# Kernel optimization log

Measured on AMD Instinct MI355X. Metric: run time of the kernel, lower is better.

## Reference

```python
import jax, jax.numpy as jnp
import numpy as np
from jax import lax

# Static config (matches init_kwargs)
D_MODEL = 1024
EXPAND = 2
D_INNER = D_MODEL * EXPAND          # 2048
HEAD_DIM = 64
N_HEADS = D_INNER // HEAD_DIM       # 32
N_GROUPS = 1
D_STATE = 128
D_CONV = 4
CONV_DIM = D_INNER + 2 * N_GROUPS * D_STATE        # 2304
D_IN_PROJ = 2 * D_INNER + 2 * N_GROUPS * D_STATE + N_HEADS  # 4384
SEQLEN = 8192
LN_EPS = 1e-5


def setup_inputs() -> dict:
    key = jax.random.key(0)
    ks = jax.random.split(key, 6)
    x = jax.random.normal(ks[0], (SEQLEN, D_MODEL), jnp.float32)
    W_in = jax.random.normal(ks[1], (D_IN_PROJ, D_MODEL), jnp.float32) / np.sqrt(D_MODEL)
    W_conv = jax.random.normal(ks[2], (CONV_DIM, 1, D_CONV), jnp.float32) / np.sqrt(D_CONV)
    b_conv = jnp.zeros((CONV_DIM,), jnp.float32)
    # dt_bias init per Mamba2: dt ~ LogUniform(dt_min, dt_max), inverse-softplus
    dt = jnp.exp(jax.random.uniform(ks[3], (N_HEADS,)) * (np.log(0.1) - np.log(0.001)) + np.log(0.001))
    dt = jnp.clip(dt, 1e-4)
    dt_bias = dt + jnp.log(-jnp.expm1(-dt))
    A_log = jnp.log(jax.random.uniform(ks[4], (N_HEADS,), minval=1.0, maxval=16.0))
    D_param = jnp.ones((N_HEADS,), jnp.float32)
    ln_w = jnp.ones((D_INNER,), jnp.float32)
    ln_b = jnp.zeros((D_INNER,), jnp.float32)
    W_out = jax.random.normal(ks[5], (D_MODEL, D_INNER), jnp.float32) / np.sqrt(D_INNER)
    return dict(x=x, W_in=W_in, W_conv=W_conv, b_conv=b_conv, dt_bias=dt_bias,
                A_log=A_log, D_param=D_param, ln_w=ln_w, ln_b=ln_b, W_out=W_out)


def reference(x, W_in, W_conv, b_conv, dt_bias, A_log, D_param, ln_w, ln_b, W_out):
    L = x.shape[0]
    zxbcdt = x @ W_in.T                                   # (L, d_in_proj)
    z = zxbcdt[:, :D_INNER]                               # gate
    xbc = zxbcdt[:, D_INNER:D_INNER + CONV_DIM]           # (L, conv_dim)
    dt = jax.nn.softplus(zxbcdt[:, D_INNER + CONV_DIM:] + dt_bias)  # (L, h)
    # depthwise causal-window conv with SAME padding over the sequence
    lhs = xbc.T[None]                                      # (1, conv_dim, L)
    conv = lax.conv_general_dilated(lhs, W_conv, (1,), 'SAME',
                                    feature_group_count=CONV_DIM,
                                    dimension_numbers=('NCH', 'OIH', 'NCH'))[0]
    xbc = jax.nn.silu((conv + b_conv[:, None]).T)          # (L, conv_dim)
    x_ssm = xbc[:, :D_INNER].reshape(L, N_HEADS, HEAD_DIM)
    B = xbc[:, D_INNER:D_INNER + N_GROUPS * D_STATE].reshape(L, N_GROUPS, D_STATE)
    C = xbc[:, D_INNER + N_GROUPS * D_STATE:].reshape(L, N_GROUPS, D_STATE)
    hpg = N_HEADS // N_GROUPS
    Bh = jnp.repeat(B, hpg, axis=1)                        # (L, h, n)
    Ch = jnp.repeat(C, hpg, axis=1)                        # (L, h, n)
    A = -jnp.exp(A_log)                                    # (h,), negative
    a = jnp.exp(dt * A)                                    # (L, h) per-token decay in (0,1)
    V = x_ssm * dt[..., None]                              # discretized input (L, h, p)
    # non-causal SSD (VSSD): global state H then readout, plus D skip
    H = jnp.einsum('lhn,lh,lhp->hnp', Bh, a, V)            # (h, n, p)
    y = jnp.einsum('lhn,hnp->lhp', Ch, H) + D_param[None, :, None] * x_ssm
    y = y.reshape(L, D_INNER)
    # LayerNorm (eqx default: weight+bias, eps=1e-5), then gate by z
    mu = jnp.mean(y, axis=-1, keepdims=True)
    var = jnp.var(y, axis=-1, keepdims=True)
    y = ((y - mu) / jnp.sqrt(var + LN_EPS)) * ln_w + ln_b
    y = y * z
    return y @ W_out.T                                     # (L, d_model)
```

## Files before the change

### kernel.cpp

```cpp
#include <hip/hip_runtime.h>
#include <hip/hip_bf16.h>
#include <math.h>

#define L_SEQ 8192
#define DM 1024
#define DI 2048
#define NH 32
#define HD 64
#define DS 128
#define CDIM 2304
#define DPROJ 4384
#define NPAD_IN 4608
#define KSPLIT 16
#define OPROWS 2176

typedef short bf16x8 __attribute__((ext_vector_type(8)));
typedef float floatx4 __attribute__((ext_vector_type(4)));
typedef unsigned short u16x4 __attribute__((ext_vector_type(4)));
typedef unsigned short u16x8 __attribute__((ext_vector_type(8)));

#define AS1(p) ((const __attribute__((address_space(1))) void*)(p))
#define AS3(p) ((__attribute__((address_space(3))) void*)(p))

__device__ __forceinline__ float bf2f(unsigned short u) {
  union { unsigned int i; float f; } c; c.i = ((unsigned int)u) << 16; return c.f;
}
__device__ __forceinline__ unsigned short f2bf(float f) {
  return __bfloat16_as_ushort(__float2bfloat16(f));
}

template <int OMODE>
__global__ __launch_bounds__(512, 2)
void gemm128_8ph(const unsigned short* __restrict__ A, int lda,
                 const unsigned short* __restrict__ B, int ldb,
                 void* __restrict__ Cout, int ldc,
                 int K, int Nstore) {
  __shared__ __align__(16) char lds[98304];
  const int t = threadIdx.x;
  const int lane = t & 63;
  const int w = t >> 6;
  const int wm = w & 1, wn = w >> 1;
  const int fr = lane & 15, quad = lane >> 4;

  int gx = gridDim.x, gy = gridDim.y;
  int linear = blockIdx.y * gx + blockIdx.x;
  int xcd = linear & 7, loc = linear >> 3;
  int mper = gy >> 3;
  int mt = xcd * mper + loc % mper;
  int nt = loc / mper;
  const int m0 = mt << 7, n0 = nt << 8;
  const int NT = K >> 6;

  floatx4 acc[4][4];
#pragma unroll
  for (int i = 0; i < 4; ++i)
#pragma unroll
    for (int j = 0; j < 4; ++j) acc[i][j] = (floatx4){0.f, 0.f, 0.f, 0.f};
  bf16x8 af[4][2], b0[2][2], b1[2][2];

  auto stA = [&](int buf, int kt) {
#pragma unroll
    for (int i = 0; i < 2; ++i) {
      int o = (i * 512 + t) * 16;
      int os = o ^ (((o >> 7) & 7) << 4);
      int rloc = os >> 7, kb = os & 127;
      const unsigned short* src = A + (size_t)(m0 + rloc) * lda + (kt << 6) + (kb >> 1);
      __builtin_amdgcn_global_load_lds(AS1(src), AS3(lds + buf * 16384 + o), 16, 0, 0);
    }
  };
  auto stB = [&](int buf, int kt, int g) {
#pragma unroll
    for (int i = 0; i < 2; ++i) {
      int o = (i * 512 + t) * 16;
      int os = o ^ (((o >> 7) & 7) << 4);
      int rloc = os >> 7, kb = os & 127;
      int R = ((rloc >> 5) << 6) | (g << 5) | (rloc & 31);
      const unsigned short* src = B + (size_t)(n0 + R) * ldb + (kt << 6) + (kb >> 1);
      __builtin_amdgcn_global_load_lds(AS1(src),
          AS3(lds + 32768 + buf * 32768 + g * 16384 + o), 16, 0, 0);
    }
  };
  auto rdA = [&](int buf, int mi, int ks) -> bf16x8 {
    int rloc = (wm << 6) | (mi << 4) | fr;
    return *(const bf16x8*)(lds + buf * 16384 + rloc * 128 +
                            (((ks << 6) | (quad << 4)) ^ ((fr & 7) << 4)));
  };
  auto rdB = [&](int buf, int ni, int ks) -> bf16x8 {
    int rloc = (wn << 5) | ((ni & 1) << 4) | fr;
    return *(const bf16x8*)(lds + 32768 + buf * 32768 + (ni >> 1) * 16384 + rloc * 128 +
                            (((ks << 6) | (quad << 4)) ^ ((fr & 7) << 4)));
  };

  stA(0, 0); stB(0, 0, 0); stB(0, 0, 1);
  if (NT > 1) {
    stA(1, 1); stB(1, 1, 0);
    asm volatile("s_waitcnt vmcnt(4)" ::: "memory");
  } else {
    asm volatile("s_waitcnt vmcnt(0)" ::: "memory");
  }
  __builtin_amdgcn_s_barrier();

  for (int kt = 0; kt < NT; ++kt) {
    const int buf = kt & 1;
    const bool pf1 = (kt + 1 < NT);
    const bool pf2 = (kt + 2 < NT);
#pragma unroll
    for (int mi = 0; mi < 4; ++mi) { af[mi][0] = rdA(buf, mi, 0); af[mi][1] = rdA(buf, mi, 1); }
#pragma unroll
    for (int ni = 0; ni < 2; ++ni) { b0[ni][0] = rdB(buf, ni, 0); b0[ni][1] = rdB(buf, ni, 1); }
    if (pf1) stB(buf ^ 1, kt + 1, 1);
    asm volatile("s_waitcnt lgkmcnt(8)" ::: "memory");
    __builtin_amdgcn_s_barrier();
    asm volatile("s_waitcnt lgkmcnt(0)" ::: "memory");
    __builtin_amdgcn_s_setprio(1);
#pragma unroll
    for (int mi = 0; mi < 4; ++mi)
#pragma unroll
      for (int ni = 0; ni < 2; ++ni)
#pragma unroll
        for (int ks = 0; ks < 2; ++ks)
          acc[mi][ni] = __builtin_amdgcn_mfma_f32_16x16x32_bf16(af[mi][ks], b0[ni][ks], acc[mi][ni], 0, 0, 0);
    __builtin_amdgcn_s_setprio(0);
    asm volatile("s_waitcnt vmcnt(6)" ::: "memory");
    __builtin_amdgcn_s_barrier();
#pragma unroll
    for (int ni = 0; ni < 2; ++ni) { b1[ni][0] = rdB(buf, ni + 2, 0); b1[ni][1] = rdB(buf, ni + 2, 1); }
    if (pf2) { stA(buf, kt + 2); stB(buf, kt + 2, 0); }
    __builtin_amdgcn_s_barrier();
    asm volatile("s_waitcnt lgkmcnt(0)" ::: "memory");
    __builtin_amdgcn_s_setprio(1);
#pragma unroll
    for (int mi = 0; mi < 4; ++mi)
#pragma unroll
      for (int ni = 0; ni < 2; ++ni)
#pragma unroll
        for (int ks = 0; ks < 2; ++ks)
          acc[mi][ni + 2] = __builtin_amdgcn_mfma_f32_16x16x32_bf16(af[mi][ks], b1[ni][ks], acc[mi][ni + 2], 0, 0, 0);
    __builtin_amdgcn_s_setprio(0);
    if (kt < NT - 1) {
      if (pf2) asm volatile("s_waitcnt vmcnt(6)" ::: "memory");
      else     asm volatile("s_waitcnt vmcnt(0)" ::: "memory");
      __builtin_amdgcn_s_barrier();
    }
  }

  if (OMODE == 0) {
    unsigned short* rp = (unsigned short*)lds;
    unsigned short* C = (unsigned short*)Cout;
    const int mb = wm * 64, nb = wn * 64;
#pragma unroll
    for (int mi = 0; mi < 4; ++mi)
#pragma unroll
      for (int ni = 0; ni < 4; ++ni)
#pragma unroll
        for (int r = 0; r < 4; ++r)
          rp[(mb + mi * 16 + quad * 4 + r) * 256 + nb + ni * 16 + fr] = f2bf(acc[mi][ni][r]);
    __syncthreads();
#pragma unroll
    for (int j = 0; j < 8; ++j) {
      int lin = j * 4096 + t * 8;
      int row = lin >> 8, col = lin & 255;
      int gcol = n0 + col;
      if (gcol < Nstore)
        *(u16x8*)&C[(size_t)(m0 + row) * ldc + gcol] = *(const u16x8*)&rp[lin];
    }
  } else {
    float* Cf = (float*)Cout;
#pragma unroll
    for (int mi = 0; mi < 4; ++mi)
#pragma unroll
      for (int ni = 0; ni < 4; ++ni) {
        int gcol = n0 + wn * 64 + ni * 16 + fr;
        int grow = m0 + wm * 64 + mi * 16 + quad * 4;
#pragma unroll
        for (int r = 0; r < 4; ++r)
          if (gcol < Nstore)
            Cf[(size_t)(grow + r) * ldc + gcol] = acc[mi][ni][r];
      }
  }
}

template <int MODE>
__global__ __launch_bounds__(256)
void gemm_bt_mfma(const unsigned short* __restrict__ A, int lda,
                  const unsigned short* __restrict__ B, int ldb,
                  void* __restrict__ Cout, int ldc,
                  int Kfull, int Nstore,
                  const unsigned short* __restrict__ xs,
                  const float* __restrict__ Dvec) {
  __shared__ __align__(16) char smem[17408];
  unsigned short* Asm = (unsigned short*)smem;
  unsigned short* Bsm = Asm + 128 * 32;
  const int t = threadIdx.x;

  int bx = blockIdx.x, by = blockIdx.y;
  if (MODE != 2) {
    int gx = gridDim.x;
    int linear = by * gx + bx;
    int xcd = linear & 7;
    int local = linear >> 3;
    by = xcd * 8 + (local & 7);
    bx = local >> 3;
  }
  const int m0 = by * 128;
  const int n0 = bx * 128;

  int kstart = 0, klen = Kfull;
  if (MODE == 2) { klen = Kfull / KSPLIT; kstart = blockIdx.z * klen; }
  const int wave = t >> 6, lane = t & 63;
  const int wm = (wave & 1) * 64;
  const int wn = (wave >> 1) * 64;
  const int fr = lane & 15;
  const int quad = lane >> 4;

  floatx4 acc[4][4];
#pragma unroll
  for (int i = 0; i < 4; ++i)
#pragma unroll
    for (int j = 0; j < 4; ++j) acc[i][j] = (floatx4){0.f, 0.f, 0.f, 0.f};

  for (int k0 = kstart; k0 < kstart + klen; k0 += 32) {
#pragma unroll
    for (int i = 0; i < 2; ++i) {
      int linear = i * 256 + t;
      int row = linear >> 2;
      int kq = (linear & 3) * 8;
      const unsigned short* ga = A + (size_t)(m0 + row) * lda + (k0 + kq);
      const unsigned short* gb = B + (size_t)(n0 + row) * ldb + (k0 + kq);
      __builtin_amdgcn_global_load_lds(AS1(ga), AS3(&Asm[linear * 8]), 16, 0, 0);
      __builtin_amdgcn_global_load_lds(AS1(gb), AS3(&Bsm[linear * 8]), 16, 0, 0);
    }
    __syncthreads();

    bf16x8 af[4], bfr[4];
#pragma unroll
    for (int i = 0; i < 4; ++i) {
      af[i]  = *(const bf16x8*)&Asm[(wm + i * 16 + fr) * 32 + quad * 8];
      bfr[i] = *(const bf16x8*)&Bsm[(wn + i * 16 + fr) * 32 + quad * 8];
    }
#pragma unroll
    for (int mi = 0; mi < 4; ++mi)
#pragma unroll
      for (int ni = 0; ni < 4; ++ni)
        acc[mi][ni] = __builtin_amdgcn_mfma_f32_16x16x32_bf16(
            af[mi], bfr[ni], acc[mi][ni], 0, 0, 0);
    __syncthreads();
  }

  const int lrbase = (wm ? 16 : 0) + quad * 4;
  if (MODE == 0 || MODE == 1) {
    unsigned short(*rp)[136] = (unsigned short(*)[136])smem;
    unsigned short* C = (unsigned short*)Cout;
#pragma unroll
    for (int mi = 0; mi < 4; ++mi) {
      __syncthreads();
#pragma unroll
      for (int ni = 0; ni < 4; ++ni)
#pragma unroll
        for (int r = 0; r < 4; ++r)
          rp[lrbase + r][wn + ni * 16 + fr] = f2bf(acc[mi][ni][r]);
      __syncthreads();
#pragma unroll
      for (int j = 0; j < 2; ++j) {
        int off = j * 2048 + t * 8;
        int lr = off >> 7, c = off & 127;
        int grow = m0 + (lr >> 4) * 64 + mi * 16 + (lr & 15);
        int gcol = n0 + c;
        u16x8 v = *(const u16x8*)&rp[lr][c];
        if (MODE == 1) {
          u16x8 xv = *(const u16x8*)&xs[(size_t)grow * ldc + gcol];
          float Dh = Dvec[gcol >> 6];
          u16x8 o;
#pragma unroll
          for (int e = 0; e < 8; ++e) o[e] = f2bf(bf2f(v[e]) + Dh * bf2f(xv[e]));
          *(u16x8*)&C[(size_t)grow * ldc + gcol] = o;
        } else {
          if (gcol < Nstore) *(u16x8*)&C[(size_t)grow * ldc + gcol] = v;
        }
      }
    }
  } else {
    float(*rpf)[136] = (float(*)[136])smem;
    float* C = (float*)Cout;
    if (MODE == 2) C += (size_t)blockIdx.z * DS * DI;
#pragma unroll
    for (int mi = 0; mi < 4; ++mi) {
      __syncthreads();
#pragma unroll
      for (int ni = 0; ni < 4; ++ni)
#pragma unroll
        for (int r = 0; r < 4; ++r)
          rpf[lrbase + r][wn + ni * 16 + fr] = acc[mi][ni][r];
      __syncthreads();
#pragma unroll
      for (int j = 0; j < 4; ++j) {
        int off = j * 1024 + t * 4;
        int lr = off >> 7, c = off & 127;
        int grow = m0 + (lr >> 4) * 64 + mi * 16 + (lr & 15);
        int gcol = n0 + c;
        float4 v = *(const float4*)&rpf[lr][c];
        *(float4*)&C[(size_t)grow * ldc + gcol] = v;
      }
    }
  }
}

__global__ __launch_bounds__(256)
void cast_all_kernel(const float* __restrict__ x, const float* __restrict__ W_in,
                     const float* __restrict__ W_out,
                     unsigned short* __restrict__ x_bf16,
                     unsigned short* __restrict__ win_bf16,
                     unsigned short* __restrict__ wout_bf16) {
  int b = blockIdx.x;
  int t = threadIdx.x;
  u16x4 o = (u16x4){0, 0, 0, 0};
  if (b < 8192) {
    size_t i4 = ((size_t)b * 256 + t) * 4;
    float4 v = *(const float4*)(x + i4);
    o.x = f2bf(v.x); o.y = f2bf(v.y); o.z = f2bf(v.z); o.w = f2bf(v.w);
    *(u16x4*)(x_bf16 + i4) = o;
  } else if (b < 12800) {
    size_t i4 = ((size_t)(b - 8192) * 256 + t) * 4;
    int row = (int)(i4 >> 10);
    if (row < DPROJ) {
      float4 v = *(const float4*)(W_in + i4);
      o.x = f2bf(v.x); o.y = f2bf(v.y); o.z = f2bf(v.z); o.w = f2bf(v.w);
    }
    *(u16x4*)(win_bf16 + i4) = o;
  } else {
    size_t i4 = ((size_t)(b - 12800) * 256 + t) * 4;
    float4 v = *(const float4*)(W_out + i4);
    o.x = f2bf(v.x); o.y = f2bf(v.y); o.z = f2bf(v.z); o.w = f2bf(v.w);
    *(u16x4*)(wout_bf16 + i4) = o;
  }
}

__global__ __launch_bounds__(256)
void dt_kernel(const unsigned short* __restrict__ zxb, const float* __restrict__ dt_bias,
               const float* __restrict__ A_log, float* __restrict__ s_out) {
  int idx = blockIdx.x * 256 + threadIdx.x;
  int l = idx >> 5, h = idx & 31;
  float v = bf2f(zxb[(size_t)l * DPROJ + (DI + CDIM) + h]) + dt_bias[h];
  float d = (v > 20.f) ? v : log1pf(expf(v));
  s_out[idx] = d * expf(-d * expf(A_log[h]));
}

__global__ __launch_bounds__(256)
void conv_fused_kernel(const unsigned short* __restrict__ zxb,
                       const float* __restrict__ Wc,
                       const float* __restrict__ bc,
                       const float* __restrict__ svec,
                       unsigned short* __restrict__ xs,
                       unsigned short* __restrict__ cb,
                       unsigned short* __restrict__ OpT) {
  __shared__ unsigned short zt[67][66];
  __shared__ unsigned short ot[64][66];
  __shared__ float sl[64];
  const int c0 = blockIdx.x * 64;
  const int l0 = blockIdx.y * 64;
  const int t = threadIdx.x;
  for (int idx = t; idx < 67 * 16; idx += 256) {
    int row = idx >> 4;
    int colq = (idx & 15) * 4;
    int gl = l0 - 1 + row;
    u16x4 v = (u16x4){0, 0, 0, 0};
    if (gl >= 0 && gl < L_SEQ)
      v = *(const u16x4*)&zxb[(size_t)gl * DPROJ + DI + c0 + colq];
    *(u16x4*)&zt[row][colq] = v;
  }
  const bool isX = (c0 < DI);
  const bool isC = (c0 >= DI + DS);
  if (isX && t < 64) sl[t] = svec[(size_t)(l0 + t) * NH + (c0 >> 6)];
  const int c = t & 63;
  const int gc = c0 + c;
  const float4 wv = *(const float4*)&Wc[gc * 4];
  const float bias = bc[gc];
  const int lq = (t >> 6) * 16;
  __syncthreads();
#pragma unroll
  for (int i = 0; i < 16; ++i) {
    int ll = lq + i;
    float sacc = bias + bf2f(zt[ll][c]) * wv.x + bf2f(zt[ll + 1][c]) * wv.y +
                 bf2f(zt[ll + 2][c]) * wv.z + bf2f(zt[ll + 3][c]) * wv.w;
    float v = sacc / (1.f + expf(-sacc));
    int gl = l0 + ll;
    if (isC) {
      cb[(size_t)gl * DS + (gc - (DI + DS))] = f2bf(v);
    } else if (isX) {
      xs[(size_t)gl * DI + gc] = f2bf(v);
      ot[c][ll] = f2bf(v * sl[ll]);
    } else {
      ot[c][ll] = f2bf(v);
    }
  }
  if (!isC) {
    __syncthreads();
#pragma unroll
    for (int j = 0; j < 4; ++j) {
      int linear = j * 1024 + t * 4;
      int rr = linear >> 6;
      int lc = linear & 63;
      *(u16x4*)&OpT[(size_t)(c0 + rr) * L_SEQ + l0 + lc] = *(const u16x4*)&ot[rr][lc];
    }
  }
}

__global__ __launch_bounds__(256)
void h_reduce_t_kernel(const float* __restrict__ P, unsigned short* __restrict__ Ht) {
  __shared__ float tile[32][65];
  const int bid = blockIdx.x;
  const int pt = bid & 31, ng = bid >> 5;
  const int t = threadIdx.x;
#pragma unroll
  for (int i = 0; i < 8; ++i) {
    int nl = i * 4 + (t >> 6);
    int n = ng * 32 + nl;
    int p = pt * 64 + (t & 63);
    float acc = 0.f;
#pragma unroll
    for (int z = 0; z < KSPLIT; ++z)
      acc += P[(size_t)z * (DS * DI) + (size_t)n * DI + p];
    tile[nl][t & 63] = acc;
  }
  __syncthreads();
#pragma unroll
  for (int j = 0; j < 8; ++j) {
    int linear = j * 256 + t;
    int pl = linear >> 5, nl = linear & 31;
    Ht[(size_t)(pt * 64 + pl) * DS + ng * 32 + nl] = f2bf(tile[nl][pl]);
  }
}

__global__ __launch_bounds__(256)
void ln_mul_kernel(const unsigned short* __restrict__ ybuf, unsigned short* __restrict__ zxb,
                   const float* __restrict__ ln_w, const float* __restrict__ ln_b) {
  int l = blockIdx.x;
  int t = threadIdx.x;
  int c0 = t * 8;
  u16x8 yv = *(const u16x8*)&ybuf[(size_t)l * DI + c0];
  float vals[8];
  float s = 0.f, sq = 0.f;
#pragma unroll
  for (int i = 0; i < 8; ++i) {
    float v = bf2f(yv[i]);
    vals[i] = v;
    s += v;
    sq += v * v;
  }
#pragma unroll
  for (int off = 32; off > 0; off >>= 1) {
    s += __shfl_down(s, off, 64);
    sq += __shfl_down(sq, off, 64);
  }
  __shared__ float red[10];
  int wave = t >> 6, lane = t & 63;
  if (lane == 0) { red[wave] = s; red[4 + wave] = sq; }
  __syncthreads();
  if (t == 0) {
    float S = red[0] + red[1] + red[2] + red[3];
    float SQ = red[4] + red[5] + red[6] + red[7];
    float mu = S / (float)DI;
    red[8] = mu;
    red[9] = rsqrtf(SQ / (float)DI - mu * mu + 1e-5f);
  }
  __syncthreads();
  float mu = red[8], rstd = red[9];
  unsigned short* zrow = zxb + (size_t)l * DPROJ;
  u16x8 zv = *(const u16x8*)&zrow[c0];
  float4 w0 = *(const float4*)&ln_w[c0], w1 = *(const float4*)&ln_w[c0 + 4];
  float4 b0 = *(const float4*)&ln_b[c0], b1 = *(const float4*)&ln_b[c0 + 4];
  float w[8] = {w0.x, w0.y, w0.z, w0.w, w1.x, w1.y, w1.z, w1.w};
  float b[8] = {b0.x, b0.y, b0.z, b0.w, b1.x, b1.y, b1.z, b1.w};
  u16x8 o;
#pragma unroll
  for (int i = 0; i < 8; ++i) {
    float v = (vals[i] - mu) * rstd * w[i] + b[i];
    o[i] = f2bf(v * bf2f(zv[i]));
  }
  *(u16x8*)&zrow[DI + c0] = o;
}

extern "C" void kernel_launch(void* const* d_in, const int* in_sizes, int n_in,
                              void* d_out, int out_size, void* d_ws, size_t ws_size,
                              hipStream_t stream) {
  const float* x       = (const float*)d_in[0];
  const float* W_in    = (const float*)d_in[1];
  const float* W_conv  = (const float*)d_in[2];
  const float* b_conv  = (const float*)d_in[3];
  const float* dt_bias = (const float*)d_in[4];
  const float* A_log   = (const float*)d_in[5];
  const float* D_param = (const float*)d_in[6];
  const float* ln_w    = (const float*)d_in[7];
  const float* ln_b    = (const float*)d_in[8];
  const float* W_out   = (const float*)d_in[9];
  float* out = (float*)d_out;

  unsigned short* zxb = (unsigned short*)d_ws;
  unsigned short* xs   = zxb + (size_t)L_SEQ * DPROJ;
  unsigned short* cb   = xs + (size_t)L_SEQ * DI;
  float* svec = (float*)(cb + (size_t)L_SEQ * DS);
  unsigned short* OpT = (unsigned short*)(svec + (size_t)L_SEQ * NH);
  float* Ppart = (float*)(OpT + (size_t)OPROWS * L_SEQ);
  unsigned short* Ht = (unsigned short*)(Ppart + (size_t)KSPLIT * DS * DI);
  unsigned short* wout_bf16 = Ht + (size_t)DI * DS;
  unsigned short* x_bf16   = OpT;
  unsigned short* win_bf16 = OpT + (size_t)L_SEQ * DM;
  unsigned short* ybuf     = OpT;

  cast_all_kernel<<<14848, 256, 0, stream>>>(x, W_in, W_out, x_bf16, win_bf16,
                                             wout_bf16);

  gemm128_8ph<0><<<dim3(NPAD_IN / 256, L_SEQ / 128), 512, 0, stream>>>(
      x_bf16, DM, win_bf16, DM, zxb, DPROJ, DM, DPROJ);

  dt_kernel<<<(L_SEQ * NH) / 256, 256, 0, stream>>>(zxb, dt_bias, A_log, svec);

  conv_fused_kernel<<<dim3(CDIM / 64, L_SEQ / 64), 256, 0, stream>>>(
      zxb, W_conv, b_conv, svec, xs, cb, OpT);

  gemm_bt_mfma<2><<<dim3(DI / 128, 1, KSPLIT), 256, 0, stream>>>(
      OpT + (size_t)DI * L_SEQ, L_SEQ, OpT, L_SEQ, Ppart, DI, L_SEQ, DI,
      nullptr, nullptr);

  h_reduce_t_kernel<<<128, 256, 0, stream>>>(Ppart, Ht);

  gemm_bt_mfma<1><<<dim3(DI / 128, L_SEQ / 128), 256, 0, stream>>>(
      cb, DS, Ht, DS, ybuf, DI, DS, DI, xs, D_param);

  ln_mul_kernel<<<L_SEQ, 256, 0, stream>>>(ybuf, zxb, ln_w, ln_b);

  gemm128_8ph<1><<<dim3(DM / 256, L_SEQ / 128), 512, 0, stream>>>(
      zxb + DI, DPROJ, wout_bf16, DI, out, DM, DI, DM);
}
```

Before: 340.2 us.

## Shrink GEMM LDS to single-buffered B ring to raise occupancy

The GEMM kernel is restructured so B is single-buffered in LDS (64KB instead of 96KB), with the B halves streamed in a ring pattern and A still double-buffered. Launch bounds are raised to allow more resident blocks per CU. The aim is better latency hiding through occupancy. The cost is a shorter prefetch distance: B for the next tile is loaded within the current iteration, and there is a full vmcnt(0) wait each iteration, which can expose memory latency.

```diff
diff --git a/kernel.cpp b/kernel.cpp
--- a/kernel.cpp
+++ b/kernel.cpp
@@ -30,12 +30,12 @@
 }
 
 template <int OMODE>
-__global__ __launch_bounds__(512, 2)
-void gemm128_8ph(const unsigned short* __restrict__ A, int lda,
-                 const unsigned short* __restrict__ B, int ldb,
-                 void* __restrict__ Cout, int ldc,
-                 int K, int Nstore) {
-  __shared__ __align__(16) char lds[98304];
+__global__ __launch_bounds__(512, 4)
+void gemm128_ring(const unsigned short* __restrict__ A, int lda,
+                  const unsigned short* __restrict__ B, int ldb,
+                  void* __restrict__ Cout, int ldc,
+                  int K, int Nstore) {
+  __shared__ __align__(16) char lds[65536];
   const int t = threadIdx.x;
   const int lane = t & 63;
   const int w = t >> 6;
@@ -68,7 +68,7 @@
       __builtin_amdgcn_global_load_lds(AS1(src), AS3(lds + buf * 16384 + o), 16, 0, 0);
     }
   };
-  auto stB = [&](int buf, int kt, int g) {
+  auto stBg = [&](int kt, int g) {
 #pragma unroll
     for (int i = 0; i < 2; ++i) {
       int o = (i * 512 + t) * 16;
@@ -77,7 +77,7 @@
       int R = ((rloc >> 5) << 6) | (g << 5) | (rloc & 31);
       const unsigned short* src = B + (size_t)(n0 + R) * ldb + (kt << 6) + (kb >> 1);
       __builtin_amdgcn_global_load_lds(AS1(src),
-          AS3(lds + 32768 + buf * 32768 + g * 16384 + o), 16, 0, 0);
+          AS3(lds + 32768 + g * 16384 + o), 16, 0, 0);
     }
   };
   auto rdA = [&](int buf, int mi, int ks) -> bf16x8 {
@@ -85,30 +85,25 @@
     return *(const bf16x8*)(lds + buf * 16384 + rloc * 128 +
                             (((ks << 6) | (quad << 4)) ^ ((fr & 7) << 4)));
   };
-  auto rdB = [&](int buf, int ni, int ks) -> bf16x8 {
+  auto rdB = [&](int ni, int ks) -> bf16x8 {
     int rloc = (wn << 5) | ((ni & 1) << 4) | fr;
-    return *(const bf16x8*)(lds + 32768 + buf * 32768 + (ni >> 1) * 16384 + rloc * 128 +
+    return *(const bf16x8*)(lds + 32768 + (ni >> 1) * 16384 + rloc * 128 +
                             (((ks << 6) | (quad << 4)) ^ ((fr & 7) << 4)));
   };
 
-  stA(0, 0); stB(0, 0, 0); stB(0, 0, 1);
-  if (NT > 1) {
-    stA(1, 1); stB(1, 1, 0);
-    asm volatile("s_waitcnt vmcnt(4)" ::: "memory");
-  } else {
-    asm volatile("s_waitcnt vmcnt(0)" ::: "memory");
-  }
+  stA(0, 0); stBg(0, 0);
+  asm volatile("s_waitcnt vmcnt(0)" ::: "memory");
   __builtin_amdgcn_s_barrier();
 
   for (int kt = 0; kt < NT; ++kt) {
     const int buf = kt & 1;
-    const bool pf1 = (kt + 1 < NT);
-    const bool pf2 = (kt + 2 < NT);
+    const bool pf = (kt + 1 < NT);
 #pragma unroll
     for (int mi = 0; mi < 4; ++mi) { af[mi][0] = rdA(buf, mi, 0); af[mi][1] = rdA(buf, mi, 1); }
 #pragma unroll
-    for (int ni = 0; ni < 2; ++ni) { b0[ni][0] = rdB(buf, ni, 0); b0[ni][1] = rdB(buf, ni, 1); }
-    if (pf1) stB(buf ^ 1, kt + 1, 1);
+    for (int ni = 0; ni < 2; ++ni) { b0[ni][0] = rdB(ni, 0); b0[ni][1] = rdB(ni, 1); }
+    stBg(kt, 1);
+    if (pf) stA(buf ^ 1, kt + 1);
     asm volatile("s_waitcnt lgkmcnt(8)" ::: "memory");
     __builtin_amdgcn_s_barrier();
     asm volatile("s_waitcnt lgkmcnt(0)" ::: "memory");
@@ -121,11 +116,12 @@
         for (int ks = 0; ks < 2; ++ks)
           acc[mi][ni] = __builtin_amdgcn_mfma_f32_16x16x32_bf16(af[mi][ks], b0[ni][ks], acc[mi][ni], 0, 0, 0);
     __builtin_amdgcn_s_setprio(0);
-    asm volatile("s_waitcnt vmcnt(6)" ::: "memory");
+    if (pf) asm volatile("s_waitcnt vmcnt(2)" ::: "memory");
+    else    asm volatile("s_waitcnt vmcnt(0)" ::: "memory");
     __builtin_amdgcn_s_barrier();
 #pragma unroll
-    for (int ni = 0; ni < 2; ++ni) { b1[ni][0] = rdB(buf, ni + 2, 0); b1[ni][1] = rdB(buf, ni + 2, 1); }
-    if (pf2) { stA(buf, kt + 2); stB(buf, kt + 2, 0); }
+    for (int ni = 0; ni < 2; ++ni) { b1[ni][0] = rdB(ni + 2, 0); b1[ni][1] = rdB(ni + 2, 1); }
+    if (pf) stBg(kt + 1, 0);
     __builtin_amdgcn_s_barrier();
     asm volatile("s_waitcnt lgkmcnt(0)" ::: "memory");
     __builtin_amdgcn_s_setprio(1);
@@ -138,13 +134,13 @@
           acc[mi][ni + 2] = __builtin_amdgcn_mfma_f32_16x16x32_bf16(af[mi][ks], b1[ni][ks], acc[mi][ni + 2], 0, 0, 0);
     __builtin_amdgcn_s_setprio(0);
     if (kt < NT - 1) {
-      if (pf2) asm volatile("s_waitcnt vmcnt(6)" ::: "memory");
-      else     asm volatile("s_waitcnt vmcnt(0)" ::: "memory");
+      asm volatile("s_waitcnt vmcnt(0)" ::: "memory");
       __builtin_amdgcn_s_barrier();
     }
   }
 
   if (OMODE == 0) {
+    __syncthreads();
     unsigned short* rp = (unsigned short*)lds;
     unsigned short* C = (unsigned short*)Cout;
     const int mb = wm * 64, nb = wn * 64;
@@ -510,7 +506,7 @@
   cast_all_kernel<<<14848, 256, 0, stream>>>(x, W_in, W_out, x_bf16, win_bf16,
                                              wout_bf16);
 
-  gemm128_8ph<0><<<dim3(NPAD_IN / 256, L_SEQ / 128), 512, 0, stream>>>(
+  gemm128_ring<0><<<dim3(NPAD_IN / 256, L_SEQ / 128), 512, 0, stream>>>(
       x_bf16, DM, win_bf16, DM, zxb, DPROJ, DM, DPROJ);
 
   dt_kernel<<<(L_SEQ * NH) / 256, 256, 0, stream>>>(zxb, dt_bias, A_log, svec);
@@ -529,6 +525,6 @@
 
   ln_mul_kernel<<<L_SEQ, 256, 0, stream>>>(ybuf, zxb, ln_w, ln_b);
 
-  gemm128_8ph<1><<<dim3(DM / 256, L_SEQ / 128), 512, 0, stream>>>(
+  gemm128_ring<1><<<dim3(DM / 256, L_SEQ / 128), 512, 0, stream>>>(
       zxb + DI, DPROJ, wout_bf16, DI, out, DM, DI, DM);
 }
```

Measured after the change: 430.8 us. 26.6% more time.
